# Kernel optimization log

Measured on AMD Instinct MI355X. Metric: run time of the kernel, lower is better.

The kernel has to match this reference:

```python
import jax, jax.numpy as jnp
import numpy as np

B, S, HID = 2, 2048, 2560
H, NOPE, ROPE, VD = 40, 64, 32, 64
QKD = NOPE + ROPE  # 96
Q_RANK, KV_RANK = 768, 256
EPS = 1e-5
SCALING = QKD ** -0.5
NEG = -1e9


def rms_norm(x, w, eps=EPS):
    xf = x.astype(jnp.float32)
    var = jnp.mean(xf * xf, axis=-1, keepdims=True)
    return (xf * jax.lax.rsqrt(var + eps)).astype(x.dtype) * w


def rotate_half(x):
    x1, x2 = jnp.split(x, 2, axis=-1)
    return jnp.concatenate([-x2, x1], axis=-1)


def setup_inputs() -> dict:
    key = jax.random.key(0)
    ks = jax.random.split(key, 8)
    # rotary tables (rope_theta = 10000), shape [S, ROPE]
    inv_freq = 1.0 / (10000.0 ** (np.arange(0, ROPE, 2, dtype=np.float32) / ROPE))
    t = np.arange(S, dtype=np.float32)
    freqs = np.outer(t, inv_freq)  # [S, ROPE/2]
    emb = np.concatenate([freqs, freqs], axis=-1)
    return {
        "hidden_states": jax.random.normal(ks[0], (B, S, HID), jnp.float32),
        "cos": jnp.asarray(np.cos(emb)),
        "sin": jnp.asarray(np.sin(emb)),
        "wq_a": jax.random.normal(ks[1], (HID, Q_RANK), jnp.float32) * 0.02,
        "q_a_ln_w": jnp.ones((Q_RANK,), jnp.float32),
        "wq_b": jax.random.normal(ks[2], (Q_RANK, H * QKD), jnp.float32) * 0.02,
        "wkv_a": jax.random.normal(ks[3], (HID, KV_RANK + ROPE), jnp.float32) * 0.02,
        "kv_a_ln_w": jnp.ones((KV_RANK,), jnp.float32),
        "wkv_b": jax.random.normal(ks[4], (KV_RANK, H * (NOPE + VD)), jnp.float32) * 0.02,
        "wo": jax.random.normal(ks[5], (H * VD, HID), jnp.float32) * 0.02,
    }


def reference(hidden_states, cos, sin, wq_a, q_a_ln_w, wq_b, wkv_a, kv_a_ln_w, wkv_b, wo):
    b, s, _ = hidden_states.shape
    # low-rank query: down-proj, RMSNorm, up-proj
    q = rms_norm(hidden_states @ wq_a, q_a_ln_w) @ wq_b  # [B,S,H*QKD]
    q = q.reshape(b, s, H, QKD).transpose(0, 2, 1, 3)  # [B,H,S,QKD]
    q_pass, q_rot = q[..., :NOPE], q[..., NOPE:]
    # compressed kv + shared rope key
    ckv = hidden_states @ wkv_a  # [B,S,KV_RANK+ROPE]
    k_c, k_rot = ckv[..., :KV_RANK], ckv[..., KV_RANK:]
    kv = rms_norm(k_c, kv_a_ln_w) @ wkv_b  # [B,S,H*(NOPE+VD)]
    kv = kv.reshape(b, s, H, NOPE + VD).transpose(0, 2, 1, 3)  # [B,H,S,NOPE+VD]
    k_pass, v = kv[..., :NOPE], kv[..., NOPE:]
    # partial RoPE (standard rotate-half), cos/sin: [S,ROPE] -> [1,1,S,ROPE]
    c = cos[None, None, :, :]
    si = sin[None, None, :, :]
    q_rot = q_rot * c + rotate_half(q_rot) * si  # [B,H,S,ROPE]
    k_rot = k_rot[:, None, :, :]  # [B,1,S,ROPE]
    k_rot = k_rot * c + rotate_half(k_rot) * si
    k_rot = jnp.broadcast_to(k_rot, (b, H, s, ROPE))
    query = jnp.concatenate([q_pass, q_rot], axis=-1)  # [B,H,S,QKD]
    key = jnp.concatenate([k_pass, k_rot], axis=-1)  # [B,H,S,QKD]
    # eager causal SDPA
    scores = jnp.einsum('bhqd,bhkd->bhqk', query, key) * SCALING
    causal = jnp.tril(jnp.ones((s, s), bool))
    scores = jnp.where(causal[None, None], scores, NEG)
    probs = jax.nn.softmax(scores.astype(jnp.float32), axis=-1).astype(query.dtype)
    out = jnp.einsum('bhqk,bhkd->bhqd', probs, v)  # [B,H,S,VD]
    out = out.transpose(0, 2, 1, 3).reshape(b, s, H * VD)
    return out @ wo
```

## Files before the change

kernel.cpp:

```cpp
#include <hip/hip_runtime.h>
#include <hip/hip_bf16.h>
#include <cstdint>

#define B_ 2
#define S_ 2048
#define HID_ 2560
#define H_ 40
#define NOPE_ 64
#define ROPE_ 32
#define VD_ 64
#define QKD_ 96
#define QRANK_ 768
#define KVRANK_ 256
#define KVRP_ 288
#define KVRP_PAD 384
#define HQKD (H_*QKD_)
#define HKV  (H_*(NOPE_+VD_))
#define HVD  (H_*VD_)
#define TOK  (B_*S_)
#define EPS_ 1e-5f
#define SCALING_ 0.10206207261596575f

typedef __bf16  bf16x8  __attribute__((ext_vector_type(8)));
typedef float   floatx4 __attribute__((ext_vector_type(4)));
typedef short   shortx4 __attribute__((ext_vector_type(4)));
typedef unsigned short ushort8_t __attribute__((ext_vector_type(8)));

__device__ __forceinline__ unsigned short f2bf(float f) {
    unsigned int u = __builtin_bit_cast(unsigned int, f);
    unsigned int r = (u + 0x7FFFu + ((u >> 16) & 1u)) >> 16;
    return (unsigned short)r;
}
__device__ __forceinline__ float bf2f(unsigned short h) {
    return __builtin_bit_cast(float, ((unsigned int)h) << 16);
}
__device__ __forceinline__ float load_in(const void* p, long i, int bf) {
    if (bf) return bf2f(((const unsigned short*)p)[i]);
    return ((const float*)p)[i];
}

__device__ __forceinline__ void gl_lds16(const unsigned short* g, unsigned short* l) {
    __builtin_amdgcn_global_load_lds(
        (const __attribute__((address_space(1))) unsigned int*)g,
        (__attribute__((address_space(3))) unsigned int*)l, 16, 0, 0);
}

__global__ void k_detect(const unsigned short* cosb, int* flag) {
    if (threadIdx.x == 0) flag[0] = (cosb[0] != 0) ? 1 : 0;
}

__global__ void k_tobf(const void* in, unsigned short* out, long n, const int* flag) {
    int bf = flag[0];
    long i = (long)blockIdx.x * blockDim.x + threadIdx.x;
    if (i >= n) return;
    out[i] = bf ? ((const unsigned short*)in)[i] : f2bf(((const float*)in)[i]);
}

__global__ __launch_bounds__(256) void k_transpose(const void* in, unsigned short* out,
                                                   int K, int N, int Npad, const int* flag) {
    __shared__ float tile[32][33];
    int bf = flag[0];
    int k0 = blockIdx.x * 32;
    int n0 = blockIdx.y * 32;
    int tx = threadIdx.x & 31, ty = threadIdx.x >> 5;
#pragma unroll
    for (int i = 0; i < 4; i++) {
        int k = k0 + ty + 8 * i, n = n0 + tx;
        float v = 0.f;
        if (n < N && k < K) v = load_in(in, (long)k * N + n, bf);
        tile[ty + 8 * i][tx] = v;
    }
    __syncthreads();
#pragma unroll
    for (int i = 0; i < 4; i++) {
        int n = n0 + ty + 8 * i, k = k0 + tx;
        if (n < Npad && k < K) out[(long)n * K + k] = f2bf(tile[tx][ty + 8 * i]);
    }
}

__global__ __launch_bounds__(256) void k_vtrans(const unsigned short* kv, unsigned short* vt) {
    __shared__ unsigned short t[32][33];
    int bh = blockIdx.z;
    int s0 = blockIdx.x * 32, v0 = blockIdx.y * 32;
    int b = bh / H_, h = bh % H_;
    int tx = threadIdx.x & 31, ty = threadIdx.x >> 5;
#pragma unroll
    for (int i = 0; i < 4; i++) {
        int s = s0 + ty + 8 * i, vd = v0 + tx;
        t[ty + 8 * i][tx] = kv[((long)b * S_ + s) * HKV + h * 128 + 64 + vd];
    }
    __syncthreads();
#pragma unroll
    for (int i = 0; i < 4; i++) {
        int vd = v0 + ty + 8 * i, s = s0 + tx;
        vt[((long)bh * 64 + vd) * S_ + s] = t[tx][ty + 8 * i];
    }
}

__global__ __launch_bounds__(256) void k_rmsnorm(const float* in, int ldin, int L,
                                                 const void* w, unsigned short* out,
                                                 int ldout, const int* flag) {
    int bf = flag[0];
    long row = blockIdx.x;
    const float* x = in + row * ldin;
    float ss = 0.f;
    for (int i = threadIdx.x; i < L; i += 256) { float v = x[i]; ss += v * v; }
    __shared__ float red[256];
    red[threadIdx.x] = ss;
    __syncthreads();
    for (int s = 128; s > 0; s >>= 1) {
        if (threadIdx.x < s) red[threadIdx.x] += red[threadIdx.x + s];
        __syncthreads();
    }
    float scale = rsqrtf(red[0] / (float)L + EPS_);
    for (int i = threadIdx.x; i < L; i += 256)
        out[row * ldout + i] = f2bf(x[i] * scale * load_in(w, i, bf));
}

__global__ void k_rope_q(unsigned short* q, const void* cosb, const void* sinb, const int* flag) {
    int bf = flag[0];
    long i = (long)blockIdx.x * blockDim.x + threadIdx.x;
    if (i >= (long)TOK * H_ * 16) return;
    int r = (int)(i & 15);
    long t = i >> 4;
    int h = (int)(t % H_);
    long tok = t / H_;
    int s = (int)(tok % S_);
    long base = tok * HQKD + h * QKD_ + NOPE_;
    float x1 = bf2f(q[base + r]), x2 = bf2f(q[base + 16 + r]);
    float c1 = load_in(cosb, (long)s * ROPE_ + r, bf);
    float s1 = load_in(sinb, (long)s * ROPE_ + r, bf);
    float c2 = load_in(cosb, (long)s * ROPE_ + 16 + r, bf);
    float s2 = load_in(sinb, (long)s * ROPE_ + 16 + r, bf);
    q[base + r]      = f2bf(x1 * c1 - x2 * s1);
    q[base + 16 + r] = f2bf(x2 * c2 + x1 * s2);
}

__global__ void k_rope_k(const float* ckv, unsigned short* krot,
                         const void* cosb, const void* sinb, const int* flag) {
    int bf = flag[0];
    long i = (long)blockIdx.x * blockDim.x + threadIdx.x;
    if (i >= (long)TOK * 16) return;
    int r = (int)(i & 15);
    long tok = i >> 4;
    int s = (int)(tok % S_);
    const float* x = ckv + tok * KVRP_PAD + KVRANK_;
    float x1 = x[r], x2 = x[16 + r];
    float c1 = load_in(cosb, (long)s * ROPE_ + r, bf);
    float s1 = load_in(sinb, (long)s * ROPE_ + r, bf);
    float c2 = load_in(cosb, (long)s * ROPE_ + 16 + r, bf);
    float s2 = load_in(sinb, (long)s * ROPE_ + 16 + r, bf);
    krot[tok * ROPE_ + r]      = f2bf(x1 * c1 - x2 * s1);
    krot[tok * ROPE_ + 16 + r] = f2bf(x2 * c2 + x1 * s2);
}

__global__ __launch_bounds__(256) void k_gemm(const unsigned short* A, const unsigned short* Bt,
                                              void* C, int M, int N, int K,
                                              int out_mode, const int* flag) {
    int obf = (out_mode == 2) ? flag[0] : out_mode;
    __shared__ __align__(16) unsigned short As[128 * 32];
    __shared__ __align__(16) unsigned short Bs[128 * 32];
    int tid = threadIdx.x;
    int gm = blockIdx.y * 128, gn = blockIdx.x * 128;
    int lane = tid & 63, w = tid >> 6, wm = w >> 1, wn = w & 1;
    int g = lane >> 4, qi = lane & 15;
    int srow = lane >> 2;
    int scol = (lane & 3) * 8;
    const unsigned short* Ag0 = A  + (long)(gm + w * 16 + srow) * K + scol;
    const unsigned short* Ag1 = A  + (long)(gm + (w + 4) * 16 + srow) * K + scol;
    const unsigned short* Bg0 = Bt + (long)(gn + w * 16 + srow) * K + scol;
    const unsigned short* Bg1 = Bt + (long)(gn + (w + 4) * 16 + srow) * K + scol;
    unsigned short* Al0 = &As[w * 512];
    unsigned short* Al1 = &As[(w + 4) * 512];
    unsigned short* Bl0 = &Bs[w * 512];
    unsigned short* Bl1 = &Bs[(w + 4) * 512];

    floatx4 acc[4][4];
#pragma unroll
    for (int mt = 0; mt < 4; mt++)
#pragma unroll
        for (int nt = 0; nt < 4; nt++) acc[mt][nt] = (floatx4){0.f, 0.f, 0.f, 0.f};

    for (int k0 = 0; k0 < K; k0 += 32) {
        __syncthreads();
        gl_lds16(Ag0 + k0, Al0);
        gl_lds16(Ag1 + k0, Al1);
        gl_lds16(Bg0 + k0, Bl0);
        gl_lds16(Bg1 + k0, Bl1);
        __syncthreads();
        bf16x8 fa[4], fb[4];
#pragma unroll
        for (int mt = 0; mt < 4; mt++) fa[mt] = *(const bf16x8*)&As[(wm * 64 + mt * 16 + qi) * 32 + g * 8];
#pragma unroll
        for (int nt = 0; nt < 4; nt++) fb[nt] = *(const bf16x8*)&Bs[(wn * 64 + nt * 16 + qi) * 32 + g * 8];
#pragma unroll
        for (int mt = 0; mt < 4; mt++)
#pragma unroll
            for (int nt = 0; nt < 4; nt++)
                acc[mt][nt] = __builtin_amdgcn_mfma_f32_16x16x32_bf16(fa[mt], fb[nt], acc[mt][nt], 0, 0, 0);
    }
#pragma unroll
    for (int mt = 0; mt < 4; mt++)
#pragma unroll
        for (int nt = 0; nt < 4; nt++)
#pragma unroll
            for (int r = 0; r < 4; r++) {
                long row = gm + wm * 64 + mt * 16 + g * 4 + r;
                long col = gn + wn * 64 + nt * 16 + qi;
                float v = acc[mt][nt][r];
                if (obf) ((unsigned short*)C)[row * N + col] = f2bf(v);
                else     ((float*)C)[row * N + col] = v;
            }
}

__global__ __launch_bounds__(256) void k_attn(const unsigned short* q, const unsigned short* kv,
                                              const unsigned short* krot, const unsigned short* vt,
                                              unsigned short* out) {
    __shared__ __align__(16) unsigned short Ks[64 * 96];
    __shared__ __align__(16) unsigned short Vs[64 * 80];
    int tid = threadIdx.x;
    int lane = tid & 63, w = tid >> 6;
    int b = blockIdx.z, h = blockIdx.y;
    int j = blockIdx.x;
    int g = lane >> 4, qi = lane & 15;
    long tok0 = (long)b * S_;

    const unsigned short* kbase = kv + tok0 * HKV + h * 128;
    const unsigned short* krb   = krot + tok0 * ROPE_;
    const unsigned short* vtb   = vt + ((long)(b * H_ + h) * 64) * S_;

    for (int half = 0; half < 2; half++) {
        int qblk = half ? (15 - j) : j;
        int qbase = qblk * 128;

        bf16x8 fq[2][3];
#pragma unroll
        for (int qt = 0; qt < 2; qt++) {
            const unsigned short* qp = q + (tok0 + qbase + w * 32 + qt * 16 + qi) * HQKD + h * QKD_;
#pragma unroll
            for (int c = 0; c < 3; c++) fq[qt][c] = *(const bf16x8*)&qp[c * 32 + g * 8];
        }

        floatx4 o[2][4];
#pragma unroll
        for (int qt = 0; qt < 2; qt++)
#pragma unroll
            for (int vc = 0; vc < 4; vc++) o[qt][vc] = (floatx4){0.f, 0.f, 0.f, 0.f};
        float m[2] = {-1e30f, -1e30f}, l[2] = {0.f, 0.f};

        int ktb = 2 * qblk + 2;
        int ktmax_w = (qbase + w * 32 + 31) >> 6;

        for (int kt = 0; kt < ktb; kt++) {
            int k0 = kt * 64;
            __syncthreads();
#pragma unroll
            for (int i = 0; i < 3; i++) {
                int idx = tid + i * 256;
                int row = idx / 12, c = (idx % 12) * 8;
                const unsigned short* src = (c < 64)
                    ? kbase + (long)(k0 + row) * HKV + c
                    : krb + (long)(k0 + row) * ROPE_ + (c - 64);
                *(ushort8_t*)&Ks[row * 96 + c] = *(const ushort8_t*)src;
            }
#pragma unroll
            for (int i = 0; i < 2; i++) {
                int idx = tid + i * 256;
                int row = idx >> 3, c = (idx & 7) * 8;
                *(ushort8_t*)&Vs[row * 80 + c] = *(const ushort8_t*)&vtb[(long)row * S_ + k0 + c];
            }
            __syncthreads();
            if (kt > ktmax_w) continue;

            floatx4 st[2][4];
#pragma unroll
            for (int kk = 0; kk < 4; kk++) {
                const unsigned short* kr = &Ks[(kk * 16 + qi) * 96];
                bf16x8 fk0 = *(const bf16x8*)&kr[g * 8];
                bf16x8 fk1 = *(const bf16x8*)&kr[32 + g * 8];
                bf16x8 fk2 = *(const bf16x8*)&kr[64 + g * 8];
#pragma unroll
                for (int qt = 0; qt < 2; qt++) {
                    floatx4 s = (floatx4){0.f, 0.f, 0.f, 0.f};
                    s = __builtin_amdgcn_mfma_f32_16x16x32_bf16(fk0, fq[qt][0], s, 0, 0, 0);
                    s = __builtin_amdgcn_mfma_f32_16x16x32_bf16(fk1, fq[qt][1], s, 0, 0, 0);
                    s = __builtin_amdgcn_mfma_f32_16x16x32_bf16(fk2, fq[qt][2], s, 0, 0, 0);
                    st[qt][kk] = s;
                }
            }

            shortx4 fp[2][4];
#pragma unroll
            for (int qt = 0; qt < 2; qt++) {
                int qrow = qbase + w * 32 + qt * 16 + qi;
                bool need_mask = (k0 + 63) > (qbase + w * 32 + qt * 16);
                float sv[4][4];
                float tmax = -3e30f;
#pragma unroll
                for (int kk = 0; kk < 4; kk++)
#pragma unroll
                    for (int r = 0; r < 4; r++) {
                        float s = st[qt][kk][r] * SCALING_;
                        if (need_mask && (k0 + kk * 16 + g * 4 + r) > qrow) s = -1e30f;
                        sv[kk][r] = s;
                        tmax = fmaxf(tmax, s);
                    }
                tmax = fmaxf(tmax, __shfl_xor(tmax, 16, 64));
                tmax = fmaxf(tmax, __shfl_xor(tmax, 32, 64));
                float mnew = fmaxf(m[qt], tmax);
                float alpha = __expf(m[qt] - mnew);
                float ps = 0.f;
#pragma unroll
                for (int kk = 0; kk < 4; kk++)
#pragma unroll
                    for (int r = 0; r < 4; r++) {
                        float p = __expf(sv[kk][r] - mnew);
                        ps += p;
                        fp[qt][kk][r] = (short)f2bf(p);
                    }
                ps += __shfl_xor(ps, 16, 64);
                ps += __shfl_xor(ps, 32, 64);
                l[qt] = l[qt] * alpha + ps;
                m[qt] = mnew;
                float ar[4];
#pragma unroll
                for (int r = 0; r < 4; r++) ar[r] = __shfl(alpha, (lane & 48) | (g * 4 + r), 64);
#pragma unroll
                for (int vc = 0; vc < 4; vc++) {
                    o[qt][vc][0] *= ar[0]; o[qt][vc][1] *= ar[1];
                    o[qt][vc][2] *= ar[2]; o[qt][vc][3] *= ar[3];
                }
            }

#pragma unroll
            for (int kk = 0; kk < 4; kk++) {
                shortx4 fv[4];
#pragma unroll
                for (int vc = 0; vc < 4; vc++)
                    fv[vc] = *(const shortx4*)&Vs[(vc * 16 + qi) * 80 + kk * 16 + g * 4];
#pragma unroll
                for (int qt = 0; qt < 2; qt++)
#pragma unroll
                    for (int vc = 0; vc < 4; vc++)
                        o[qt][vc] = __builtin_amdgcn_mfma_f32_16x16x16bf16_1k(fp[qt][kk], fv[vc], o[qt][vc], 0, 0, 0);
            }
        }

#pragma unroll
        for (int qt = 0; qt < 2; qt++) {
            float lr[4];
#pragma unroll
            for (int r = 0; r < 4; r++) lr[r] = __shfl(l[qt], (lane & 48) | (g * 4 + r), 64);
#pragma unroll
            for (int vc = 0; vc < 4; vc++)
#pragma unroll
                for (int r = 0; r < 4; r++)
                    out[(tok0 + qbase + w * 32 + qt * 16 + g * 4 + r) * HVD + h * VD_ + vc * 16 + qi] =
                        f2bf(o[qt][vc][r] / lr[r]);
        }
    }
}

extern "C" void kernel_launch(void* const* d_in, const int* in_sizes, int n_in,
                              void* d_out, int out_size, void* d_ws, size_t ws_size,
                              hipStream_t stream) {
    const void* hidden = d_in[0];
    const void* cosb   = d_in[1];
    const void* sinb   = d_in[2];
    const void* wq_a   = d_in[3];
    const void* q_ln   = d_in[4];
    const void* wq_b   = d_in[5];
    const void* wkv_a  = d_in[6];
    const void* kv_ln  = d_in[7];
    const void* wkv_b  = d_in[8];
    const void* wo     = d_in[9];

    char* ws = (char*)d_ws;
    size_t off = 0;
    auto alloc = [&](size_t bytes) -> void* {
        void* p = ws + off;
        off += (bytes + 255) & ~(size_t)255;
        return p;
    };
    int* flag                = (int*)alloc(256);
    unsigned short* hbf      = (unsigned short*)alloc((size_t)TOK * HID_ * 2);
    unsigned short* wqa_t    = (unsigned short*)alloc((size_t)QRANK_ * HID_ * 2);
    unsigned short* wqb_t    = (unsigned short*)alloc((size_t)HQKD * QRANK_ * 2);
    unsigned short* wkva_t   = (unsigned short*)alloc((size_t)KVRP_PAD * HID_ * 2);
    unsigned short* wkvb_t   = (unsigned short*)alloc((size_t)HKV * KVRANK_ * 2);
    unsigned short* wo_t     = (unsigned short*)alloc((size_t)HID_ * HVD * 2);
    float*          q_a      = (float*)alloc((size_t)TOK * QRANK_ * 4);
    unsigned short* q_a_n    = (unsigned short*)alloc((size_t)TOK * QRANK_ * 2);
    unsigned short* q_raw    = (unsigned short*)alloc((size_t)TOK * HQKD * 2);
    float*          ckv      = (float*)alloc((size_t)TOK * KVRP_PAD * 4);
    unsigned short* kc_n     = (unsigned short*)alloc((size_t)TOK * KVRANK_ * 2);
    unsigned short* kv_raw   = (unsigned short*)alloc((size_t)TOK * HKV * 2);
    unsigned short* krot     = (unsigned short*)alloc((size_t)TOK * ROPE_ * 2);
    unsigned short* attn_o   = (unsigned short*)alloc((size_t)TOK * HVD * 2);
    unsigned short* vt       = hbf;

    k_detect<<<1, 64, 0, stream>>>((const unsigned short*)cosb, flag);

    long nh = (long)TOK * HID_;
    k_tobf<<<(int)((nh + 255) / 256), 256, 0, stream>>>(hidden, hbf, nh, flag);

    k_transpose<<<dim3(HID_ / 32, QRANK_ / 32), 256, 0, stream>>>(wq_a, wqa_t, HID_, QRANK_, QRANK_, flag);
    k_transpose<<<dim3(QRANK_ / 32, HQKD / 32), 256, 0, stream>>>(wq_b, wqb_t, QRANK_, HQKD, HQKD, flag);
    k_transpose<<<dim3(HID_ / 32, KVRP_PAD / 32), 256, 0, stream>>>(wkv_a, wkva_t, HID_, KVRP_, KVRP_PAD, flag);
    k_transpose<<<dim3(KVRANK_ / 32, HKV / 32), 256, 0, stream>>>(wkv_b, wkvb_t, KVRANK_, HKV, HKV, flag);
    k_transpose<<<dim3(HVD / 32, HID_ / 32), 256, 0, stream>>>(wo, wo_t, HVD, HID_, HID_, flag);

    k_gemm<<<dim3(QRANK_ / 128, TOK / 128), 256, 0, stream>>>(hbf, wqa_t, q_a, TOK, QRANK_, HID_, 0, flag);
    k_rmsnorm<<<TOK, 256, 0, stream>>>(q_a, QRANK_, QRANK_, q_ln, q_a_n, QRANK_, flag);
    k_gemm<<<dim3(HQKD / 128, TOK / 128), 256, 0, stream>>>(q_a_n, wqb_t, q_raw, TOK, HQKD, QRANK_, 1, flag);

    k_gemm<<<dim3(KVRP_PAD / 128, TOK / 128), 256, 0, stream>>>(hbf, wkva_t, ckv, TOK, KVRP_PAD, HID_, 0, flag);
    k_rmsnorm<<<TOK, 256, 0, stream>>>(ckv, KVRP_PAD, KVRANK_, kv_ln, kc_n, KVRANK_, flag);
    k_gemm<<<dim3(HKV / 128, TOK / 128), 256, 0, stream>>>(kc_n, wkvb_t, kv_raw, TOK, HKV, KVRANK_, 1, flag);

    long nrq = (long)TOK * H_ * 16;
    k_rope_q<<<(int)((nrq + 255) / 256), 256, 0, stream>>>(q_raw, cosb, sinb, flag);
    long nrk = (long)TOK * 16;
    k_rope_k<<<(int)((nrk + 255) / 256), 256, 0, stream>>>(ckv, krot, cosb, sinb, flag);

    k_vtrans<<<dim3(S_ / 32, VD_ / 32, B_ * H_), 256, 0, stream>>>(kv_raw, vt);
    k_attn<<<dim3(S_ / 256, H_, B_), 256, 0, stream>>>(q_raw, kv_raw, krot, vt, attn_o);

    k_gemm<<<dim3(HID_ / 128, TOK / 128), 256, 0, stream>>>(attn_o, wo_t, d_out, TOK, HID_, HVD, 2, flag);
}
```

Before: 723.3 us.

## Double-buffer K/V tiles in attention with async global-to-LDS loads and exp2 softmax

Attention K tiles are now double-buffered in LDS and loaded with direct global-to-LDS copies (gl_lds16), while V for the next tile is prefetched into registers. This lets loads for tile kt+1 overlap with compute on tile kt and removes one barrier per iteration. The softmax now uses exp2 with a log2e-folded scale, and skips the output rescale when no lane's running max increased. It doubles LDS use per block, which may lower occupancy, and it depends on a gl_lds16 helper defined elsewhere.

```diff
diff --git a/kernel.cpp b/kernel.cpp
--- a/kernel.cpp
+++ b/kernel.cpp
@@ -20,6 +20,7 @@
 #define TOK  (B_*S_)
 #define EPS_ 1e-5f
 #define SCALING_ 0.10206207261596575f
+#define SCALE2_ 0.14724506012928484f
 
 typedef __bf16  bf16x8  __attribute__((ext_vector_type(8)));
 typedef float   floatx4 __attribute__((ext_vector_type(4)));
@@ -216,8 +217,8 @@
 __global__ __launch_bounds__(256) void k_attn(const unsigned short* q, const unsigned short* kv,
                                               const unsigned short* krot, const unsigned short* vt,
                                               unsigned short* out) {
-    __shared__ __align__(16) unsigned short Ks[64 * 96];
-    __shared__ __align__(16) unsigned short Vs[64 * 80];
+    __shared__ __align__(16) unsigned short Ks[2][64 * 96];
+    __shared__ __align__(16) unsigned short Vs[2][64 * 80];
     int tid = threadIdx.x;
     int lane = tid & 63, w = tid >> 6;
     int b = blockIdx.z, h = blockIdx.y;
@@ -229,9 +230,30 @@
     const unsigned short* krb   = krot + tok0 * ROPE_;
     const unsigned short* vtb   = vt + ((long)(b * H_ + h) * 64) * S_;
 
+    const unsigned short* ksrc0[3];
+    int kstride[3];
+#pragma unroll
+    for (int i = 0; i < 3; i++) {
+        int chunk = (w * 3 + i) * 64 + lane;
+        int row = chunk / 12, cc = (chunk % 12) * 8;
+        if (cc < 64) { ksrc0[i] = kbase + (long)row * HKV + cc;          kstride[i] = HKV; }
+        else         { ksrc0[i] = krb   + (long)row * ROPE_ + (cc - 64); kstride[i] = ROPE_; }
+    }
+    const unsigned short* vsrc0[2];
+    int vdst[2];
+#pragma unroll
+    for (int i = 0; i < 2; i++) {
+        int idx = i * 256 + tid;
+        int row = idx >> 3, cc = (idx & 7) * 8;
+        vsrc0[i] = vtb + (long)row * S_ + cc;
+        vdst[i] = row * 80 + cc;
+    }
+
     for (int half = 0; half < 2; half++) {
         int qblk = half ? (15 - j) : j;
         int qbase = qblk * 128;
+        int ktb = 2 * qblk + 2;
+        int ktmax_w = (qbase + w * 32 + 31) >> 6;
 
         bf16x8 fq[2][3];
 #pragma unroll
@@ -248,101 +270,106 @@
             for (int vc = 0; vc < 4; vc++) o[qt][vc] = (floatx4){0.f, 0.f, 0.f, 0.f};
         float m[2] = {-1e30f, -1e30f}, l[2] = {0.f, 0.f};
 
-        int ktb = 2 * qblk + 2;
-        int ktmax_w = (qbase + w * 32 + 31) >> 6;
+        __syncthreads();
+#pragma unroll
+        for (int i = 0; i < 3; i++) gl_lds16(ksrc0[i], &Ks[0][(w * 3 + i) * 512]);
+        ushort8_t vr0 = *(const ushort8_t*)vsrc0[0];
+        ushort8_t vr1 = *(const ushort8_t*)vsrc0[1];
 
         for (int kt = 0; kt < ktb; kt++) {
-            int k0 = kt * 64;
+            int p = kt & 1, np = p ^ 1;
+            *(ushort8_t*)&Vs[p][vdst[0]] = vr0;
+            *(ushort8_t*)&Vs[p][vdst[1]] = vr1;
             __syncthreads();
-#pragma unroll
-            for (int i = 0; i < 3; i++) {
-                int idx = tid + i * 256;
-                int row = idx / 12, c = (idx % 12) * 8;
-                const unsigned short* src = (c < 64)
-                    ? kbase + (long)(k0 + row) * HKV + c
-                    : krb + (long)(k0 + row) * ROPE_ + (c - 64);
-                *(ushort8_t*)&Ks[row * 96 + c] = *(const ushort8_t*)src;
+            if (kt + 1 < ktb) {
+                long k1 = (long)(kt + 1) * 64;
+#pragma unroll
+                for (int i = 0; i < 3; i++)
+                    gl_lds16(ksrc0[i] + k1 * kstride[i], &Ks[np][(w * 3 + i) * 512]);
+                vr0 = *(const ushort8_t*)(vsrc0[0] + k1);
+                vr1 = *(const ushort8_t*)(vsrc0[1] + k1);
             }
-#pragma unroll
-            for (int i = 0; i < 2; i++) {
-                int idx = tid + i * 256;
-                int row = idx >> 3, c = (idx & 7) * 8;
-                *(ushort8_t*)&Vs[row * 80 + c] = *(const ushort8_t*)&vtb[(long)row * S_ + k0 + c];
-            }
-            __syncthreads();
-            if (kt > ktmax_w) continue;
-
-            floatx4 st[2][4];
-#pragma unroll
-            for (int kk = 0; kk < 4; kk++) {
-                const unsigned short* kr = &Ks[(kk * 16 + qi) * 96];
-                bf16x8 fk0 = *(const bf16x8*)&kr[g * 8];
-                bf16x8 fk1 = *(const bf16x8*)&kr[32 + g * 8];
-                bf16x8 fk2 = *(const bf16x8*)&kr[64 + g * 8];
+            if (kt <= ktmax_w) {
+                int k0 = kt * 64;
+                const unsigned short* Kp = &Ks[p][0];
+                const unsigned short* Vp = &Vs[p][0];
+
+                floatx4 st[2][4];
+#pragma unroll
+                for (int kk = 0; kk < 4; kk++) {
+                    const unsigned short* kr = &Kp[(kk * 16 + qi) * 96];
+                    bf16x8 fk0 = *(const bf16x8*)&kr[g * 8];
+                    bf16x8 fk1 = *(const bf16x8*)&kr[32 + g * 8];
+                    bf16x8 fk2 = *(const bf16x8*)&kr[64 + g * 8];
+#pragma unroll
+                    for (int qt = 0; qt < 2; qt++) {
+                        floatx4 s = (floatx4){0.f, 0.f, 0.f, 0.f};
+                        s = __builtin_amdgcn_mfma_f32_16x16x32_bf16(fk0, fq[qt][0], s, 0, 0, 0);
+                        s = __builtin_amdgcn_mfma_f32_16x16x32_bf16(fk1, fq[qt][1], s, 0, 0, 0);
+                        s = __builtin_amdgcn_mfma_f32_16x16x32_bf16(fk2, fq[qt][2], s, 0, 0, 0);
+                        st[qt][kk] = s;
+                    }
+                }
+
+                shortx4 fp[2][4];
 #pragma unroll
                 for (int qt = 0; qt < 2; qt++) {
-                    floatx4 s = (floatx4){0.f, 0.f, 0.f, 0.f};
-                    s = __builtin_amdgcn_mfma_f32_16x16x32_bf16(fk0, fq[qt][0], s, 0, 0, 0);
-                    s = __builtin_amdgcn_mfma_f32_16x16x32_bf16(fk1, fq[qt][1], s, 0, 0, 0);
-                    s = __builtin_amdgcn_mfma_f32_16x16x32_bf16(fk2, fq[qt][2], s, 0, 0, 0);
-                    st[qt][kk] = s;
+                    int qrow = qbase + w * 32 + qt * 16 + qi;
+                    bool need_mask = (k0 + 63) > (qbase + w * 32 + qt * 16);
+                    float sv[4][4];
+                    float tmax = -3e30f;
+#pragma unroll
+                    for (int kk = 0; kk < 4; kk++)
+#pragma unroll
+                        for (int r = 0; r < 4; r++) {
+                            float s = st[qt][kk][r] * SCALE2_;
+                            if (need_mask && (k0 + kk * 16 + g * 4 + r) > qrow) s = -1e30f;
+                            sv[kk][r] = s;
+                            tmax = fmaxf(tmax, s);
+                        }
+                    tmax = fmaxf(tmax, __shfl_xor(tmax, 16, 64));
+                    tmax = fmaxf(tmax, __shfl_xor(tmax, 32, 64));
+                    float mnew = fmaxf(m[qt], tmax);
+                    float ps = 0.f;
+#pragma unroll
+                    for (int kk = 0; kk < 4; kk++)
+#pragma unroll
+                        for (int r = 0; r < 4; r++) {
+                            float pv = exp2f(sv[kk][r] - mnew);
+                            ps += pv;
+                            fp[qt][kk][r] = (short)f2bf(pv);
+                        }
+                    ps += __shfl_xor(ps, 16, 64);
+                    ps += __shfl_xor(ps, 32, 64);
+                    if (__any(mnew > m[qt])) {
+                        float alpha = exp2f(m[qt] - mnew);
+                        float ar[4];
+#pragma unroll
+                        for (int r = 0; r < 4; r++) ar[r] = __shfl(alpha, (lane & 48) | (g * 4 + r), 64);
+#pragma unroll
+                        for (int vc = 0; vc < 4; vc++) {
+                            o[qt][vc][0] *= ar[0]; o[qt][vc][1] *= ar[1];
+                            o[qt][vc][2] *= ar[2]; o[qt][vc][3] *= ar[3];
+                        }
+                        l[qt] = l[qt] * alpha + ps;
+                    } else {
+                        l[qt] += ps;
+                    }
+                    m[qt] = mnew;
                 }
-            }
-
-            shortx4 fp[2][4];
-#pragma unroll
-            for (int qt = 0; qt < 2; qt++) {
-                int qrow = qbase + w * 32 + qt * 16 + qi;
-                bool need_mask = (k0 + 63) > (qbase + w * 32 + qt * 16);
-                float sv[4][4];
-                float tmax = -3e30f;
-#pragma unroll
-                for (int kk = 0; kk < 4; kk++)
-#pragma unroll
-                    for (int r = 0; r < 4; r++) {
-                        float s = st[qt][kk][r] * SCALING_;
-                        if (need_mask && (k0 + kk * 16 + g * 4 + r) > qrow) s = -1e30f;
-                        sv[kk][r] = s;
-                        tmax = fmaxf(tmax, s);
-                    }
-                tmax = fmaxf(tmax, __shfl_xor(tmax, 16, 64));
-                tmax = fmaxf(tmax, __shfl_xor(tmax, 32, 64));
-                float mnew = fmaxf(m[qt], tmax);
-                float alpha = __expf(m[qt] - mnew);
-                float ps = 0.f;
-#pragma unroll
-                for (int kk = 0; kk < 4; kk++)
-#pragma unroll
-                    for (int r = 0; r < 4; r++) {
-                        float p = __expf(sv[kk][r] - mnew);
-                        ps += p;
-                        fp[qt][kk][r] = (short)f2bf(p);
-                    }
-                ps += __shfl_xor(ps, 16, 64);
-                ps += __shfl_xor(ps, 32, 64);
-                l[qt] = l[qt] * alpha + ps;
-                m[qt] = mnew;
-                float ar[4];
-#pragma unroll
-                for (int r = 0; r < 4; r++) ar[r] = __shfl(alpha, (lane & 48) | (g * 4 + r), 64);
-#pragma unroll
-                for (int vc = 0; vc < 4; vc++) {
-                    o[qt][vc][0] *= ar[0]; o[qt][vc][1] *= ar[1];
-                    o[qt][vc][2] *= ar[2]; o[qt][vc][3] *= ar[3];
+
+#pragma unroll
+                for (int kk = 0; kk < 4; kk++) {
+                    shortx4 fv[4];
+#pragma unroll
+                    for (int vc = 0; vc < 4; vc++)
+                        fv[vc] = *(const shortx4*)&Vp[(vc * 16 + qi) * 80 + kk * 16 + g * 4];
+#pragma unroll
+                    for (int qt = 0; qt < 2; qt++)
+#pragma unroll
+                        for (int vc = 0; vc < 4; vc++)
+                            o[qt][vc] = __builtin_amdgcn_mfma_f32_16x16x16bf16_1k(fp[qt][kk], fv[vc], o[qt][vc], 0, 0, 0);
                 }
-            }
-
-#pragma unroll
-            for (int kk = 0; kk < 4; kk++) {
-                shortx4 fv[4];
-#pragma unroll
-                for (int vc = 0; vc < 4; vc++)
-                    fv[vc] = *(const shortx4*)&Vs[(vc * 16 + qi) * 80 + kk * 16 + g * 4];
-#pragma unroll
-                for (int qt = 0; qt < 2; qt++)
-#pragma unroll
-                    for (int vc = 0; vc < 4; vc++)
-                        o[qt][vc] = __builtin_amdgcn_mfma_f32_16x16x16bf16_1k(fp[qt][kk], fv[vc], o[qt][vc], 0, 0, 0);
             }
         }
 
```

Result: slower. 786.2 us (+8.7%).
